# Optimization experiments

Measured on AMD Instinct MI355X. Metric: run time of the kernel, lower is better.

## Reference

```python
import jax, jax.numpy as jnp
import numpy as np

B, N, D, H = 32, 128, 64, 8
DH = D // H  # 8
LN_EPS = 1e-5


def _layer_norm(x, g, b):
    m = jnp.mean(x, axis=-1, keepdims=True)
    v = jnp.mean(jnp.square(x - m), axis=-1, keepdims=True)
    return (x - m) * jax.lax.rsqrt(v + LN_EPS) * g + b


def setup_inputs() -> dict:
    key = jax.random.key(0)
    ks = jax.random.split(key, 16)
    s = 0.05
    return {
        "h": jax.random.normal(ks[0], (B, N, D), jnp.float32),
        "p": jax.random.normal(ks[1], (B, N, D), jnp.float32),
        "e": jax.random.normal(ks[2], (B, N, N, D), jnp.float32),
        "k_RW": jax.random.uniform(ks[3], (B, N, N), jnp.float32),
        # projection weights stored as [in, out] (x @ W == torch Linear)
        "Wq": jax.random.normal(ks[4], (D, D), jnp.float32) * s,
        "Wk": jax.random.normal(ks[5], (D, D), jnp.float32) * s,
        "We": jax.random.normal(ks[6], (D, D), jnp.float32) * s,
        "Wv": jax.random.normal(ks[7], (D, D), jnp.float32) * s,
        "Wo": jax.random.normal(ks[8], (D, D), jnp.float32) * s,
        "bo": jnp.zeros((D,), jnp.float32),
        "ln1_g": jnp.ones((D,), jnp.float32),
        "ln1_b": jnp.zeros((D,), jnp.float32),
        "W1": jax.random.normal(ks[9], (D, 2 * D), jnp.float32) * s,
        "b1": jnp.zeros((2 * D,), jnp.float32),
        "W2": jax.random.normal(ks[10], (2 * D, D), jnp.float32) * s,
        "b2": jnp.zeros((D,), jnp.float32),
        "ln2_g": jnp.ones((D,), jnp.float32),
        "ln2_b": jnp.zeros((D,), jnp.float32),
    }


def reference(h, p, e, k_RW, Wq, Wk, We, Wv, Wo, bo, ln1_g, ln1_b, W1, b1, W2, b2, ln2_g, ln2_b):
    b, n, _ = h.shape
    Qh = (h @ Wq).reshape(b, n, H, DH)
    Kh = (h @ Wk).reshape(b, n, H, DH) * (DH ** -0.5)
    Vh = (h @ Wv).reshape(b, n, H, DH).transpose(0, 2, 1, 3)  # [b,h,n,d]
    E = (e @ We).reshape(b, n, n, H, DH)
    # edge-modulated scores: [b,h,i,j]
    scores = jnp.einsum('bihk,bjhk,bijhk->bhij', Qh, Kh, E)
    scores = jnp.exp(jnp.clip(scores, -5.0, 5.0))
    scores = scores * k_RW[:, None]  # adaptive edge PE scaling
    denom = jnp.maximum(scores.sum(-1, keepdims=True), 1e-6)
    attn = (scores @ Vh) / denom  # [b,h,n,d]
    attn = attn.transpose(0, 2, 1, 3).reshape(b, n, H * DH)
    h1 = h + (attn @ Wo + bo)  # residual + O projection
    h1 = _layer_norm(h1, ln1_g, ln1_b)
    ff = jax.nn.relu(h1 @ W1 + b1) @ W2 + b2
    h2 = _layer_norm(h1 + ff, ln2_g, ln2_b)
    return h2
```

## Files before the change

kernel.cpp:

```cpp
#include <hip/hip_runtime.h>


#define NB 32
#define NN 128
#define ND 64

typedef __attribute__((ext_vector_type(8))) __bf16 bf16x8;
typedef __attribute__((ext_vector_type(8))) unsigned short u16x8;
typedef __attribute__((ext_vector_type(4))) float f32x4;

static __device__ __forceinline__ unsigned short f2bf(float x) {
  unsigned u = __float_as_uint(x);
  u += 0x7fffu + ((u >> 16) & 1u);
  return (unsigned short)(u >> 16);
}

#define DPP_ADD(v, ctrl) \
  ((v) + __int_as_float(__builtin_amdgcn_update_dpp(0, __float_as_int(v), (ctrl), 0xf, 0xf, true)))

static __device__ __forceinline__ float wsum64(float v) {
  v += __shfl_xor(v, 1, 64);
  v += __shfl_xor(v, 2, 64);
  v += __shfl_xor(v, 4, 64);
  v += __shfl_xor(v, 8, 64);
  v += __shfl_xor(v, 16, 64);
  v += __shfl_xor(v, 32, 64);
  return v;
}

__global__ __launch_bounds__(64) void qkv_kernel(
    const float* __restrict__ h, const float* __restrict__ Wq,
    const float* __restrict__ Wk, const float* __restrict__ Wv,
    float* __restrict__ Q, float* __restrict__ K, float* __restrict__ V) {
  const int r = blockIdx.x;
  const int t = threadIdx.x;
  __shared__ float hrow[ND];
  hrow[t] = h[(size_t)r * ND + t];
  __syncthreads();
  float q = 0.f, k = 0.f, v = 0.f;
#pragma unroll 8
  for (int d = 0; d < ND; ++d) {
    const float hv = hrow[d];
    q = fmaf(hv, Wq[d * ND + t], q);
    k = fmaf(hv, Wk[d * ND + t], k);
    v = fmaf(hv, Wv[d * ND + t], v);
  }
  Q[(size_t)r * ND + t] = q;
  K[(size_t)r * ND + t] = k * 0.35355339059327373f;
  V[(size_t)r * ND + t] = v;
}

__global__ __launch_bounds__(256) void fused_kernel(
    const float* __restrict__ h, const float* __restrict__ e,
    const float* __restrict__ kRW, const float* __restrict__ We,
    const float* __restrict__ Wo, const float* __restrict__ bo,
    const float* __restrict__ g1, const float* __restrict__ be1,
    const float* __restrict__ W1, const float* __restrict__ b1,
    const float* __restrict__ W2, const float* __restrict__ b2,
    const float* __restrict__ g2, const float* __restrict__ be2,
    const float* __restrict__ Q, const float* __restrict__ K,
    const float* __restrict__ V, float* __restrict__ out) {
  const int blk = blockIdx.x;
  const int b = blk >> 7;
  const int i = blk & 127;
  const int tid = threadIdx.x;
  const int w = tid >> 6;
  const int L = tid & 63;
  const int quad = L >> 4;
  const int lrow = L & 15;

  __shared__ __align__(16) unsigned short e_lds[NN * 72];
  __shared__ __align__(16) unsigned short weT[ND * 72];
  __shared__ float S_lds[NN * 9];
  __shared__ float krw_lds[NN];
  __shared__ float q_lds[ND];
  __shared__ float partN[4 * ND];
  __shared__ float partD[4 * ND];
  __shared__ float attn_lds[ND];
  __shared__ float n1_lds[ND];
  __shared__ float ff_lds[2 * ND];

  const size_t row = (size_t)b * NN + i;
  const float* e_bi = e + row * (NN * ND);
  const size_t kvbase = (size_t)b * NN * ND;

  {
    const int c = tid & 15;
    const int r0 = tid >> 4;
#pragma unroll
    for (int p = 0; p < 8; ++p) {
      const int rr = p * 16 + r0;
      const float4 vv = *(const float4*)(e_bi + rr * ND + c * 4);
      ushort4 sv = make_ushort4(f2bf(vv.x), f2bf(vv.y), f2bf(vv.z), f2bf(vv.w));
      *(ushort4*)(&e_lds[rr * 72 + c * 4]) = sv;
    }
  }
#pragma unroll
  for (int p = 0; p < 16; ++p) {
    const int idx = p * 256 + tid;
    const int kk = idx >> 6;
    const int nn = idx & 63;
    weT[nn * 72 + kk] = f2bf(We[idx]);
  }
  if (tid < NN) krw_lds[tid] = kRW[row * NN + tid];
  if (tid < ND) q_lds[tid] = Q[row * ND + tid];
  __syncthreads();

  f32x4 acc[2][4];
#pragma unroll
  for (int mr = 0; mr < 2; ++mr)
#pragma unroll
    for (int n0 = 0; n0 < 4; ++n0) acc[mr][n0] = (f32x4){0.f, 0.f, 0.f, 0.f};

#pragma unroll
  for (int mr = 0; mr < 2; ++mr) {
    const int m0 = w * 2 + mr;
#pragma unroll
    for (int ks = 0; ks < 2; ++ks) {
      const bf16x8 av = __builtin_bit_cast(
          bf16x8, *(const u16x8*)(&e_lds[(m0 * 16 + lrow) * 72 + ks * 32 + quad * 8]));
#pragma unroll
      for (int n0 = 0; n0 < 4; ++n0) {
        const bf16x8 bv = __builtin_bit_cast(
            bf16x8, *(const u16x8*)(&weT[(n0 * 16 + lrow) * 72 + ks * 32 + quad * 8]));
        acc[mr][n0] = __builtin_amdgcn_mfma_f32_16x16x32_bf16(av, bv, acc[mr][n0], 0, 0, 0);
      }
    }
  }

#pragma unroll
  for (int mr = 0; mr < 2; ++mr) {
    const int m0 = w * 2 + mr;
#pragma unroll
    for (int n0 = 0; n0 < 4; ++n0) {
      const int dout = n0 * 16 + lrow;
      const int hh = dout >> 3;
      const float qv = q_lds[dout];
      float sv[4];
#pragma unroll
      for (int reg = 0; reg < 4; ++reg) {
        const int j = m0 * 16 + quad * 4 + reg;
        const float kv = K[kvbase + (size_t)j * ND + dout];
        float tv = acc[mr][n0][reg] * qv * kv;
        tv = DPP_ADD(tv, 0xB1);
        tv = DPP_ADD(tv, 0x4E);
        tv = DPP_ADD(tv, 0x141);
        sv[reg] = __expf(fminf(fmaxf(tv, -5.f), 5.f)) * krw_lds[j];
      }
      if ((L & 7) == 0) {
#pragma unroll
        for (int reg = 0; reg < 4; ++reg)
          S_lds[(m0 * 16 + quad * 4 + reg) * 9 + hh] = sv[reg];
      }
    }
  }
  __syncthreads();

  {
    float nump = 0.f, denp = 0.f;
#pragma unroll 4
    for (int jj = 0; jj < 32; ++jj) {
      const int j = w * 32 + jj;
      const float s = S_lds[j * 9 + (L >> 3)];
      const float v = V[kvbase + (size_t)j * ND + L];
      nump = fmaf(s, v, nump);
      denp += s;
    }
    partN[w * ND + L] = nump;
    partD[w * ND + L] = denp;
  }
  __syncthreads();

  if (tid >= 64) return;
  const int t = tid;
  const float num = partN[t] + partN[64 + t] + partN[128 + t] + partN[192 + t];
  const float den = partD[t] + partD[64 + t] + partD[128 + t] + partD[192 + t];
  attn_lds[t] = num / fmaxf(den, 1e-6f);
  __builtin_amdgcn_wave_barrier();

  float o = bo[t];
#pragma unroll 8
  for (int d = 0; d < ND; ++d) o = fmaf(attn_lds[d], Wo[d * ND + t], o);
  const float h1 = h[row * ND + t] + o;

  const float m1 = wsum64(h1) * (1.f / 64.f);
  const float df1 = h1 - m1;
  const float v1 = wsum64(df1 * df1) * (1.f / 64.f);
  const float n1 = df1 * rsqrtf(v1 + 1e-5f) * g1[t] + be1[t];
  n1_lds[t] = n1;
  __builtin_amdgcn_wave_barrier();

  float a0 = b1[t], a1 = b1[64 + t];
#pragma unroll 8
  for (int d = 0; d < ND; ++d) {
    const float nv = n1_lds[d];
    a0 = fmaf(nv, W1[d * 128 + t], a0);
    a1 = fmaf(nv, W1[d * 128 + 64 + t], a1);
  }
  ff_lds[t] = fmaxf(a0, 0.f);
  ff_lds[64 + t] = fmaxf(a1, 0.f);
  __builtin_amdgcn_wave_barrier();

  float o2 = b2[t];
#pragma unroll 8
  for (int u = 0; u < 128; ++u) o2 = fmaf(ff_lds[u], W2[u * ND + t], o2);
  const float x = n1 + o2;

  const float m2 = wsum64(x) * (1.f / 64.f);
  const float df2 = x - m2;
  const float v2 = wsum64(df2 * df2) * (1.f / 64.f);
  out[row * ND + t] = df2 * rsqrtf(v2 + 1e-5f) * g2[t] + be2[t];
}

extern "C" void kernel_launch(void* const* d_in, const int* in_sizes, int n_in,
                              void* d_out, int out_size, void* d_ws, size_t ws_size,
                              hipStream_t stream) {
  const float* h   = (const float*)d_in[0];
  const float* e   = (const float*)d_in[2];
  const float* kRW = (const float*)d_in[3];
  const float* Wq  = (const float*)d_in[4];
  const float* Wk  = (const float*)d_in[5];
  const float* We  = (const float*)d_in[6];
  const float* Wv  = (const float*)d_in[7];
  const float* Wo  = (const float*)d_in[8];
  const float* bo  = (const float*)d_in[9];
  const float* g1  = (const float*)d_in[10];
  const float* be1 = (const float*)d_in[11];
  const float* W1  = (const float*)d_in[12];
  const float* b1  = (const float*)d_in[13];
  const float* W2  = (const float*)d_in[14];
  const float* b2  = (const float*)d_in[15];
  const float* g2  = (const float*)d_in[16];
  const float* be2 = (const float*)d_in[17];
  float* out = (float*)d_out;

  float* Q = (float*)d_ws;
  float* K = Q + (size_t)NB * NN * ND;
  float* V = K + (size_t)NB * NN * ND;

  qkv_kernel<<<NB * NN, 64, 0, stream>>>(h, Wq, Wk, Wv, Q, K, V);
  fused_kernel<<<NB * NN, 256, 0, stream>>>(h, e, kRW, We, Wo, bo, g1, be1,
                                            W1, b1, W2, b2, g2, be2, Q, K, V, out);
}
```

Before: 284.3 us.

## Load edge MFMA fragments directly to registers and precompute bf16 We transpose

The edge tile is now read from global memory straight into MFMA A-fragments in registers, so the e_lds staging buffer and its barrier go away. The We weight is converted to a bf16 transposed copy once by an extra block in the QKV kernel, and each block loads its B-fragments from that copy. The serial single-wave tail (O projection, FFN and LayerNorms) is split across all four waves with partial sums in LDS, and launch bounds request higher occupancy. This trades LDS use and tail latency for more barriers and possibly less coalesced global reads of e.

```diff
diff --git a/kernel.cpp b/kernel.cpp
--- a/kernel.cpp
+++ b/kernel.cpp
@@ -31,7 +31,20 @@
 __global__ __launch_bounds__(64) void qkv_kernel(
     const float* __restrict__ h, const float* __restrict__ Wq,
     const float* __restrict__ Wk, const float* __restrict__ Wv,
-    float* __restrict__ Q, float* __restrict__ K, float* __restrict__ V) {
+    const float* __restrict__ We,
+    float* __restrict__ Q, float* __restrict__ K, float* __restrict__ V,
+    unsigned short* __restrict__ WeT) {
+  if (blockIdx.x == NB * NN) {
+    const int t = threadIdx.x;
+#pragma unroll
+    for (int k0 = 0; k0 < ND; k0 += 8) {
+      u16x8 u;
+#pragma unroll
+      for (int j = 0; j < 8; ++j) u[j] = f2bf(We[(k0 + j) * ND + t]);
+      *(u16x8*)(&WeT[t * ND + k0]) = u;
+    }
+    return;
+  }
   const int r = blockIdx.x;
   const int t = threadIdx.x;
   __shared__ float hrow[ND];
@@ -50,16 +63,17 @@
   V[(size_t)r * ND + t] = v;
 }
 
-__global__ __launch_bounds__(256) void fused_kernel(
+__global__ __launch_bounds__(256, 4) void fused_kernel(
     const float* __restrict__ h, const float* __restrict__ e,
-    const float* __restrict__ kRW, const float* __restrict__ We,
+    const float* __restrict__ kRW,
     const float* __restrict__ Wo, const float* __restrict__ bo,
     const float* __restrict__ g1, const float* __restrict__ be1,
     const float* __restrict__ W1, const float* __restrict__ b1,
     const float* __restrict__ W2, const float* __restrict__ b2,
     const float* __restrict__ g2, const float* __restrict__ be2,
     const float* __restrict__ Q, const float* __restrict__ K,
-    const float* __restrict__ V, float* __restrict__ out) {
+    const float* __restrict__ V, const unsigned short* __restrict__ WeT,
+    float* __restrict__ out) {
   const int blk = blockIdx.x;
   const int b = blk >> 7;
   const int i = blk & 127;
@@ -69,8 +83,6 @@
   const int quad = L >> 4;
   const int lrow = L & 15;
 
-  __shared__ __align__(16) unsigned short e_lds[NN * 72];
-  __shared__ __align__(16) unsigned short weT[ND * 72];
   __shared__ float S_lds[NN * 9];
   __shared__ float krw_lds[NN];
   __shared__ float q_lds[ND];
@@ -84,49 +96,47 @@
   const float* e_bi = e + row * (NN * ND);
   const size_t kvbase = (size_t)b * NN * ND;
 
-  {
-    const int c = tid & 15;
-    const int r0 = tid >> 4;
-#pragma unroll
-    for (int p = 0; p < 8; ++p) {
-      const int rr = p * 16 + r0;
-      const float4 vv = *(const float4*)(e_bi + rr * ND + c * 4);
-      ushort4 sv = make_ushort4(f2bf(vv.x), f2bf(vv.y), f2bf(vv.z), f2bf(vv.w));
-      *(ushort4*)(&e_lds[rr * 72 + c * 4]) = sv;
-    }
-  }
-#pragma unroll
-  for (int p = 0; p < 16; ++p) {
-    const int idx = p * 256 + tid;
-    const int kk = idx >> 6;
-    const int nn = idx & 63;
-    weT[nn * 72 + kk] = f2bf(We[idx]);
-  }
   if (tid < NN) krw_lds[tid] = kRW[row * NN + tid];
   if (tid < ND) q_lds[tid] = Q[row * ND + tid];
-  __syncthreads();
+
+  bf16x8 a_frag[2][2];
+#pragma unroll
+  for (int mr = 0; mr < 2; ++mr) {
+    const int jrow = (w * 2 + mr) * 16 + lrow;
+#pragma unroll
+    for (int ks = 0; ks < 2; ++ks) {
+      const float* p = e_bi + jrow * ND + ks * 32 + quad * 8;
+      const float4 v0 = *(const float4*)(p);
+      const float4 v1 = *(const float4*)(p + 4);
+      u16x8 u;
+      u[0] = f2bf(v0.x); u[1] = f2bf(v0.y); u[2] = f2bf(v0.z); u[3] = f2bf(v0.w);
+      u[4] = f2bf(v1.x); u[5] = f2bf(v1.y); u[6] = f2bf(v1.z); u[7] = f2bf(v1.w);
+      a_frag[mr][ks] = __builtin_bit_cast(bf16x8, u);
+    }
+  }
+  bf16x8 b_frag[2][4];
+#pragma unroll
+  for (int ks = 0; ks < 2; ++ks)
+#pragma unroll
+    for (int n0 = 0; n0 < 4; ++n0)
+      b_frag[ks][n0] = __builtin_bit_cast(
+          bf16x8, *(const u16x8*)(&WeT[(n0 * 16 + lrow) * ND + ks * 32 + quad * 8]));
 
   f32x4 acc[2][4];
 #pragma unroll
   for (int mr = 0; mr < 2; ++mr)
 #pragma unroll
     for (int n0 = 0; n0 < 4; ++n0) acc[mr][n0] = (f32x4){0.f, 0.f, 0.f, 0.f};
-
-#pragma unroll
-  for (int mr = 0; mr < 2; ++mr) {
-    const int m0 = w * 2 + mr;
-#pragma unroll
-    for (int ks = 0; ks < 2; ++ks) {
-      const bf16x8 av = __builtin_bit_cast(
-          bf16x8, *(const u16x8*)(&e_lds[(m0 * 16 + lrow) * 72 + ks * 32 + quad * 8]));
-#pragma unroll
-      for (int n0 = 0; n0 < 4; ++n0) {
-        const bf16x8 bv = __builtin_bit_cast(
-            bf16x8, *(const u16x8*)(&weT[(n0 * 16 + lrow) * 72 + ks * 32 + quad * 8]));
-        acc[mr][n0] = __builtin_amdgcn_mfma_f32_16x16x32_bf16(av, bv, acc[mr][n0], 0, 0, 0);
-      }
-    }
-  }
+#pragma unroll
+  for (int mr = 0; mr < 2; ++mr)
+#pragma unroll
+    for (int ks = 0; ks < 2; ++ks)
+#pragma unroll
+      for (int n0 = 0; n0 < 4; ++n0)
+        acc[mr][n0] = __builtin_amdgcn_mfma_f32_16x16x32_bf16(
+            a_frag[mr][ks], b_frag[ks][n0], acc[mr][n0], 0, 0, 0);
+
+  __syncthreads();
 
 #pragma unroll
   for (int mr = 0; mr < 2; ++mr) {
@@ -171,45 +181,68 @@
   }
   __syncthreads();
 
-  if (tid >= 64) return;
-  const int t = tid;
-  const float num = partN[t] + partN[64 + t] + partN[128 + t] + partN[192 + t];
-  const float den = partD[t] + partD[64 + t] + partD[128 + t] + partD[192 + t];
-  attn_lds[t] = num / fmaxf(den, 1e-6f);
-  __builtin_amdgcn_wave_barrier();
-
-  float o = bo[t];
-#pragma unroll 8
-  for (int d = 0; d < ND; ++d) o = fmaf(attn_lds[d], Wo[d * ND + t], o);
-  const float h1 = h[row * ND + t] + o;
-
-  const float m1 = wsum64(h1) * (1.f / 64.f);
-  const float df1 = h1 - m1;
-  const float v1 = wsum64(df1 * df1) * (1.f / 64.f);
-  const float n1 = df1 * rsqrtf(v1 + 1e-5f) * g1[t] + be1[t];
-  n1_lds[t] = n1;
-  __builtin_amdgcn_wave_barrier();
-
-  float a0 = b1[t], a1 = b1[64 + t];
-#pragma unroll 8
-  for (int d = 0; d < ND; ++d) {
-    const float nv = n1_lds[d];
-    a0 = fmaf(nv, W1[d * 128 + t], a0);
-    a1 = fmaf(nv, W1[d * 128 + 64 + t], a1);
-  }
-  ff_lds[t] = fmaxf(a0, 0.f);
-  ff_lds[64 + t] = fmaxf(a1, 0.f);
-  __builtin_amdgcn_wave_barrier();
-
-  float o2 = b2[t];
-#pragma unroll 8
-  for (int u = 0; u < 128; ++u) o2 = fmaf(ff_lds[u], W2[u * ND + t], o2);
-  const float x = n1 + o2;
-
-  const float m2 = wsum64(x) * (1.f / 64.f);
-  const float df2 = x - m2;
-  const float v2 = wsum64(df2 * df2) * (1.f / 64.f);
-  out[row * ND + t] = df2 * rsqrtf(v2 + 1e-5f) * g2[t] + be2[t];
+  if (tid < ND) {
+    const float num = partN[tid] + partN[64 + tid] + partN[128 + tid] + partN[192 + tid];
+    const float den = partD[tid] + partD[64 + tid] + partD[128 + tid] + partD[192 + tid];
+    attn_lds[tid] = num / fmaxf(den, 1e-6f);
+  }
+  __syncthreads();
+
+  {
+    float po = 0.f;
+#pragma unroll
+    for (int dd = 0; dd < 16; ++dd) {
+      const int d = w * 16 + dd;
+      po = fmaf(attn_lds[d], Wo[d * ND + L], po);
+    }
+    partN[w * ND + L] = po;
+  }
+  __syncthreads();
+  if (tid < ND) {
+    const float o = bo[tid] + partN[tid] + partN[64 + tid] + partN[128 + tid] + partN[192 + tid];
+    const float h1 = h[row * ND + tid] + o;
+    const float m1 = wsum64(h1) * (1.f / 64.f);
+    const float df1 = h1 - m1;
+    const float v1 = wsum64(df1 * df1) * (1.f / 64.f);
+    n1_lds[tid] = df1 * rsqrtf(v1 + 1e-5f) * g1[tid] + be1[tid];
+  }
+  __syncthreads();
+
+  {
+    const int ch = tid & 127;
+    const int half = tid >> 7;
+    float a = 0.f;
+#pragma unroll
+    for (int dd = 0; dd < 32; ++dd) {
+      const int d = half * 32 + dd;
+      a = fmaf(n1_lds[d], W1[d * 128 + ch], a);
+    }
+    partD[half * 128 + ch] = a;
+  }
+  __syncthreads();
+  if (tid < 128) ff_lds[tid] = fmaxf(b1[tid] + partD[tid] + partD[128 + tid], 0.f);
+  __syncthreads();
+
+  {
+    const int ch = tid & 63;
+    const int q = tid >> 6;
+    float a = 0.f;
+#pragma unroll
+    for (int uu = 0; uu < 32; ++uu) {
+      const int u = q * 32 + uu;
+      a = fmaf(ff_lds[u], W2[u * ND + ch], a);
+    }
+    partN[q * ND + ch] = a;
+  }
+  __syncthreads();
+  if (tid < ND) {
+    const float x = n1_lds[tid] + b2[tid] +
+                    partN[tid] + partN[64 + tid] + partN[128 + tid] + partN[192 + tid];
+    const float m2 = wsum64(x) * (1.f / 64.f);
+    const float df2 = x - m2;
+    const float v2 = wsum64(df2 * df2) * (1.f / 64.f);
+    out[row * ND + tid] = df2 * rsqrtf(v2 + 1e-5f) * g2[tid] + be2[tid];
+  }
 }
 
 extern "C" void kernel_launch(void* const* d_in, const int* in_sizes, int n_in,
@@ -237,8 +270,9 @@
   float* Q = (float*)d_ws;
   float* K = Q + (size_t)NB * NN * ND;
   float* V = K + (size_t)NB * NN * ND;
-
-  qkv_kernel<<<NB * NN, 64, 0, stream>>>(h, Wq, Wk, Wv, Q, K, V);
-  fused_kernel<<<NB * NN, 256, 0, stream>>>(h, e, kRW, We, Wo, bo, g1, be1,
-                                            W1, b1, W2, b2, g2, be2, Q, K, V, out);
-}
+  unsigned short* WeT = (unsigned short*)(V + (size_t)NB * NN * ND);
+
+  qkv_kernel<<<NB * NN + 1, 64, 0, stream>>>(h, Wq, Wk, Wv, We, Q, K, V, WeT);
+  fused_kernel<<<NB * NN, 256, 0, stream>>>(h, e, kRW, Wo, bo, g1, be1,
+                                            W1, b1, W2, b2, g2, be2, Q, K, V, WeT, out);
+}
```

Result: faster. 261.7 us (-7.9%).

## Single-wave fused block loading e directly into MFMA registers, pretransposed We and K

Applied to the files above, without the earlier changes.

The fused kernel moves from four waves per (b,i) row to one wave. That wave streams e straight from global memory into bf16 MFMA A-fragments instead of staging it in LDS. We is converted to bf16 and transposed once, in an extra block of the QKV kernel, so each block no longer rebuilds it. K is stored transposed so score computation can read it with float4 loads. This removes LDS staging, the per-block We transpose and the cross-wave partial-sum reduction, but leaves one wave per block to handle the 32KB e tile and the serial V loop, which reduces latency hiding per block.

```diff
diff --git a/kernel.cpp b/kernel.cpp
--- a/kernel.cpp
+++ b/kernel.cpp
@@ -31,7 +31,20 @@
 __global__ __launch_bounds__(64) void qkv_kernel(
     const float* __restrict__ h, const float* __restrict__ Wq,
     const float* __restrict__ Wk, const float* __restrict__ Wv,
-    float* __restrict__ Q, float* __restrict__ K, float* __restrict__ V) {
+    const float* __restrict__ We,
+    float* __restrict__ Q, float* __restrict__ KT, float* __restrict__ V,
+    unsigned short* __restrict__ WeT) {
+  if (blockIdx.x == NB * NN) {
+    const int t = threadIdx.x;
+#pragma unroll
+    for (int k0 = 0; k0 < ND; k0 += 8) {
+      u16x8 u;
+#pragma unroll
+      for (int j = 0; j < 8; ++j) u[j] = f2bf(We[(k0 + j) * ND + t]);
+      *(u16x8*)(&WeT[t * ND + k0]) = u;
+    }
+    return;
+  }
   const int r = blockIdx.x;
   const int t = threadIdx.x;
   __shared__ float hrow[ND];
@@ -46,36 +59,32 @@
     v = fmaf(hv, Wv[d * ND + t], v);
   }
   Q[(size_t)r * ND + t] = q;
-  K[(size_t)r * ND + t] = k * 0.35355339059327373f;
+  KT[((size_t)(r >> 7) * ND + t) * NN + (r & 127)] = k * 0.35355339059327373f;
   V[(size_t)r * ND + t] = v;
 }
 
-__global__ __launch_bounds__(256) void fused_kernel(
+__global__ __launch_bounds__(64, 4) void fused_kernel(
     const float* __restrict__ h, const float* __restrict__ e,
-    const float* __restrict__ kRW, const float* __restrict__ We,
+    const float* __restrict__ kRW,
     const float* __restrict__ Wo, const float* __restrict__ bo,
     const float* __restrict__ g1, const float* __restrict__ be1,
     const float* __restrict__ W1, const float* __restrict__ b1,
     const float* __restrict__ W2, const float* __restrict__ b2,
     const float* __restrict__ g2, const float* __restrict__ be2,
-    const float* __restrict__ Q, const float* __restrict__ K,
-    const float* __restrict__ V, float* __restrict__ out) {
+    const float* __restrict__ Q, const float* __restrict__ KT,
+    const float* __restrict__ V, const unsigned short* __restrict__ WeT,
+    float* __restrict__ out) {
   const int blk = blockIdx.x;
   const int b = blk >> 7;
   const int i = blk & 127;
-  const int tid = threadIdx.x;
-  const int w = tid >> 6;
-  const int L = tid & 63;
+  const int L = threadIdx.x;
   const int quad = L >> 4;
   const int lrow = L & 15;
-
-  __shared__ __align__(16) unsigned short e_lds[NN * 72];
-  __shared__ __align__(16) unsigned short weT[ND * 72];
+  const int h8 = L >> 3;
+
   __shared__ float S_lds[NN * 9];
   __shared__ float krw_lds[NN];
   __shared__ float q_lds[ND];
-  __shared__ float partN[4 * ND];
-  __shared__ float partD[4 * ND];
   __shared__ float attn_lds[ND];
   __shared__ float n1_lds[ND];
   __shared__ float ff_lds[2 * ND];
@@ -83,133 +92,109 @@
   const size_t row = (size_t)b * NN + i;
   const float* e_bi = e + row * (NN * ND);
   const size_t kvbase = (size_t)b * NN * ND;
-
-  {
-    const int c = tid & 15;
-    const int r0 = tid >> 4;
-#pragma unroll
-    for (int p = 0; p < 8; ++p) {
-      const int rr = p * 16 + r0;
-      const float4 vv = *(const float4*)(e_bi + rr * ND + c * 4);
-      ushort4 sv = make_ushort4(f2bf(vv.x), f2bf(vv.y), f2bf(vv.z), f2bf(vv.w));
-      *(ushort4*)(&e_lds[rr * 72 + c * 4]) = sv;
+  const size_t ktbase = (size_t)b * ND * NN;
+
+  q_lds[L] = Q[row * ND + L];
+  krw_lds[L] = kRW[row * NN + L];
+  krw_lds[64 + L] = kRW[row * NN + 64 + L];
+
+  bf16x8 bfr[2][4];
+#pragma unroll
+  for (int ks = 0; ks < 2; ++ks)
+#pragma unroll
+    for (int n0 = 0; n0 < 4; ++n0)
+      bfr[ks][n0] = __builtin_bit_cast(
+          bf16x8, *(const u16x8*)(&WeT[(n0 * 16 + lrow) * ND + ks * 32 + quad * 8]));
+
+  __syncthreads();
+
+#pragma unroll 2
+  for (int mr = 0; mr < 8; ++mr) {
+    const float* p = e_bi + (mr * 16 + lrow) * ND;
+    bf16x8 afr[2];
+#pragma unroll
+    for (int ks = 0; ks < 2; ++ks) {
+      const float4 v0 = *(const float4*)(p + ks * 32 + quad * 8);
+      const float4 v1 = *(const float4*)(p + ks * 32 + quad * 8 + 4);
+      u16x8 u;
+      u[0] = f2bf(v0.x); u[1] = f2bf(v0.y); u[2] = f2bf(v0.z); u[3] = f2bf(v0.w);
+      u[4] = f2bf(v1.x); u[5] = f2bf(v1.y); u[6] = f2bf(v1.z); u[7] = f2bf(v1.w);
+      afr[ks] = __builtin_bit_cast(bf16x8, u);
     }
-  }
-#pragma unroll
-  for (int p = 0; p < 16; ++p) {
-    const int idx = p * 256 + tid;
-    const int kk = idx >> 6;
-    const int nn = idx & 63;
-    weT[nn * 72 + kk] = f2bf(We[idx]);
-  }
-  if (tid < NN) krw_lds[tid] = kRW[row * NN + tid];
-  if (tid < ND) q_lds[tid] = Q[row * ND + tid];
-  __syncthreads();
-
-  f32x4 acc[2][4];
-#pragma unroll
-  for (int mr = 0; mr < 2; ++mr)
-#pragma unroll
-    for (int n0 = 0; n0 < 4; ++n0) acc[mr][n0] = (f32x4){0.f, 0.f, 0.f, 0.f};
-
-#pragma unroll
-  for (int mr = 0; mr < 2; ++mr) {
-    const int m0 = w * 2 + mr;
-#pragma unroll
-    for (int ks = 0; ks < 2; ++ks) {
-      const bf16x8 av = __builtin_bit_cast(
-          bf16x8, *(const u16x8*)(&e_lds[(m0 * 16 + lrow) * 72 + ks * 32 + quad * 8]));
-#pragma unroll
-      for (int n0 = 0; n0 < 4; ++n0) {
-        const bf16x8 bv = __builtin_bit_cast(
-            bf16x8, *(const u16x8*)(&weT[(n0 * 16 + lrow) * 72 + ks * 32 + quad * 8]));
-        acc[mr][n0] = __builtin_amdgcn_mfma_f32_16x16x32_bf16(av, bv, acc[mr][n0], 0, 0, 0);
-      }
-    }
-  }
-
-#pragma unroll
-  for (int mr = 0; mr < 2; ++mr) {
-    const int m0 = w * 2 + mr;
+    f32x4 acc[4];
+#pragma unroll
+    for (int n0 = 0; n0 < 4; ++n0) acc[n0] = (f32x4){0.f, 0.f, 0.f, 0.f};
+#pragma unroll
+    for (int ks = 0; ks < 2; ++ks)
+#pragma unroll
+      for (int n0 = 0; n0 < 4; ++n0)
+        acc[n0] = __builtin_amdgcn_mfma_f32_16x16x32_bf16(afr[ks], bfr[ks][n0], acc[n0], 0, 0, 0);
+
 #pragma unroll
     for (int n0 = 0; n0 < 4; ++n0) {
       const int dout = n0 * 16 + lrow;
-      const int hh = dout >> 3;
       const float qv = q_lds[dout];
+      const float4 kv = *(const float4*)(&KT[ktbase + (size_t)dout * NN + mr * 16 + quad * 4]);
+      const float* kvp = (const float*)&kv;
       float sv[4];
 #pragma unroll
       for (int reg = 0; reg < 4; ++reg) {
-        const int j = m0 * 16 + quad * 4 + reg;
-        const float kv = K[kvbase + (size_t)j * ND + dout];
-        float tv = acc[mr][n0][reg] * qv * kv;
+        float tv = acc[n0][reg] * qv * kvp[reg];
         tv = DPP_ADD(tv, 0xB1);
         tv = DPP_ADD(tv, 0x4E);
         tv = DPP_ADD(tv, 0x141);
-        sv[reg] = __expf(fminf(fmaxf(tv, -5.f), 5.f)) * krw_lds[j];
+        sv[reg] = __expf(fminf(fmaxf(tv, -5.f), 5.f)) * krw_lds[mr * 16 + quad * 4 + reg];
       }
       if ((L & 7) == 0) {
 #pragma unroll
         for (int reg = 0; reg < 4; ++reg)
-          S_lds[(m0 * 16 + quad * 4 + reg) * 9 + hh] = sv[reg];
+          S_lds[(mr * 16 + quad * 4 + reg) * 9 + (dout >> 3)] = sv[reg];
       }
     }
   }
   __syncthreads();
 
-  {
-    float nump = 0.f, denp = 0.f;
-#pragma unroll 4
-    for (int jj = 0; jj < 32; ++jj) {
-      const int j = w * 32 + jj;
-      const float s = S_lds[j * 9 + (L >> 3)];
-      const float v = V[kvbase + (size_t)j * ND + L];
-      nump = fmaf(s, v, nump);
-      denp += s;
-    }
-    partN[w * ND + L] = nump;
-    partD[w * ND + L] = denp;
-  }
-  __syncthreads();
-
-  if (tid >= 64) return;
-  const int t = tid;
-  const float num = partN[t] + partN[64 + t] + partN[128 + t] + partN[192 + t];
-  const float den = partD[t] + partD[64 + t] + partD[128 + t] + partD[192 + t];
-  attn_lds[t] = num / fmaxf(den, 1e-6f);
-  __builtin_amdgcn_wave_barrier();
-
-  float o = bo[t];
-#pragma unroll 8
-  for (int d = 0; d < ND; ++d) o = fmaf(attn_lds[d], Wo[d * ND + t], o);
-  const float h1 = h[row * ND + t] + o;
-
-  const float m1 = wsum64(h1) * (1.f / 64.f);
-  const float df1 = h1 - m1;
+  float nump = 0.f, denp = 0.f;
+#pragma unroll 8
+  for (int j = 0; j < NN; ++j) {
+    const float s = S_lds[j * 9 + h8];
+    const float v = V[kvbase + (size_t)j * ND + L];
+    nump = fmaf(s, v, nump);
+    denp += s;
+  }
+  attn_lds[L] = nump / fmaxf(denp, 1e-6f);
+  __syncthreads();
+
+  float o = bo[L];
+#pragma unroll 8
+  for (int d = 0; d < ND; ++d) o = fmaf(attn_lds[d], Wo[d * ND + L], o);
+  const float h1v = h[row * ND + L] + o;
+  const float m1 = wsum64(h1v) * (1.f / 64.f);
+  const float df1 = h1v - m1;
   const float v1 = wsum64(df1 * df1) * (1.f / 64.f);
-  const float n1 = df1 * rsqrtf(v1 + 1e-5f) * g1[t] + be1[t];
-  n1_lds[t] = n1;
-  __builtin_amdgcn_wave_barrier();
-
-  float a0 = b1[t], a1 = b1[64 + t];
+  const float n1 = df1 * rsqrtf(v1 + 1e-5f) * g1[L] + be1[L];
+  n1_lds[L] = n1;
+  __syncthreads();
+
+  float a0 = b1[L], a1 = b1[64 + L];
 #pragma unroll 8
   for (int d = 0; d < ND; ++d) {
     const float nv = n1_lds[d];
-    a0 = fmaf(nv, W1[d * 128 + t], a0);
-    a1 = fmaf(nv, W1[d * 128 + 64 + t], a1);
-  }
-  ff_lds[t] = fmaxf(a0, 0.f);
-  ff_lds[64 + t] = fmaxf(a1, 0.f);
-  __builtin_amdgcn_wave_barrier();
-
-  float o2 = b2[t];
-#pragma unroll 8
-  for (int u = 0; u < 128; ++u) o2 = fmaf(ff_lds[u], W2[u * ND + t], o2);
+    a0 = fmaf(nv, W1[d * 128 + L], a0);
+    a1 = fmaf(nv, W1[d * 128 + 64 + L], a1);
+  }
+  ff_lds[L] = fmaxf(a0, 0.f);
+  ff_lds[64 + L] = fmaxf(a1, 0.f);
+  __syncthreads();
+
+  float o2 = b2[L];
+#pragma unroll 8
+  for (int u = 0; u < 128; ++u) o2 = fmaf(ff_lds[u], W2[u * ND + L], o2);
   const float x = n1 + o2;
-
   const float m2 = wsum64(x) * (1.f / 64.f);
   const float df2 = x - m2;
   const float v2 = wsum64(df2 * df2) * (1.f / 64.f);
-  out[row * ND + t] = df2 * rsqrtf(v2 + 1e-5f) * g2[t] + be2[t];
+  out[row * ND + L] = df2 * rsqrtf(v2 + 1e-5f) * g2[L] + be2[L];
 }
 
 extern "C" void kernel_launch(void* const* d_in, const int* in_sizes, int n_in,
@@ -234,11 +219,12 @@
   const float* be2 = (const float*)d_in[17];
   float* out = (float*)d_out;
 
-  float* Q = (float*)d_ws;
-  float* K = Q + (size_t)NB * NN * ND;
-  float* V = K + (size_t)NB * NN * ND;
-
-  qkv_kernel<<<NB * NN, 64, 0, stream>>>(h, Wq, Wk, Wv, Q, K, V);
-  fused_kernel<<<NB * NN, 256, 0, stream>>>(h, e, kRW, We, Wo, bo, g1, be1,
-                                            W1, b1, W2, b2, g2, be2, Q, K, V, out);
-}
+  float* Q  = (float*)d_ws;
+  float* KT = Q + (size_t)NB * NN * ND;
+  float* V  = KT + (size_t)NB * NN * ND;
+  unsigned short* WeT = (unsigned short*)(V + (size_t)NB * NN * ND);
+
+  qkv_kernel<<<NB * NN + 1, 64, 0, stream>>>(h, Wq, Wk, Wv, We, Q, KT, V, WeT);
+  fused_kernel<<<NB * NN, 64, 0, stream>>>(h, e, kRW, Wo, bo, g1, be1,
+                                           W1, b1, W2, b2, g2, be2, Q, KT, V, WeT, out);
+}
```

After: 258.0 us. 9.2% less time.
